# Kernel optimization log

Measured on AMD Instinct MI355X. Metric: run time of the kernel, lower is better.

Reference implementation:

```python
import jax, jax.numpy as jnp
import numpy as np

B, S, DIM = 2, 2048, 2048
NH, NKV = 16, 8
HD = DIM // NH  # 128
ROPE_THETA = 10000.0


def setup_inputs() -> dict:
    key = jax.random.key(0)
    ks = jax.random.split(key, 7)
    std = DIM ** -0.5
    x = jax.random.normal(ks[0], (B, S, DIM), jnp.float32)
    wq = jax.random.normal(ks[1], (NH * HD, DIM), jnp.float32) * std
    wk = jax.random.normal(ks[2], (NKV * HD, DIM), jnp.float32) * std
    wv = jax.random.normal(ks[3], (NKV * HD, DIM), jnp.float32) * std
    wo = jax.random.normal(ks[4], (DIM, NH * HD), jnp.float32) * std
    inv_freq = 1.0 / (ROPE_THETA ** (jnp.arange(0, HD, 2, dtype=jnp.float32) / HD))
    ang = jnp.arange(S, dtype=jnp.float32)[:, None] * inv_freq[None, :]  # [S, HD//2]
    freqs_cos = jnp.cos(ang)
    freqs_sin = jnp.sin(ang)
    # diffusion-style random per-batch token mask: t ~ U[0,1) per batch row
    t = jax.random.uniform(ks[5], (B, 1))
    mask = jax.random.uniform(ks[6], (B, S)) < t  # True = masked key
    mask = mask.at[:, 0].set(False)  # first token never masked
    return dict(x=x, wq=wq, wk=wk, wv=wv, wo=wo,
                freqs_cos=freqs_cos, freqs_sin=freqs_sin, mask=mask)


def _rope(x, cos, sin):
    # x: [b, s, h, d]; pairs (x[2i], x[2i+1]) rotated by angle[s, i]
    xr, xi = x[..., 0::2], x[..., 1::2]
    c = cos[None, :, None, :]
    s = sin[None, :, None, :]
    out = jnp.stack([xr * c - xi * s, xr * s + xi * c], axis=-1)
    return out.reshape(x.shape)


def reference(x, wq, wk, wv, wo, freqs_cos, freqs_sin, mask):
    b, s, _ = x.shape
    xq = jnp.einsum('bsd,ed->bse', x, wq).reshape(b, s, NH, HD)
    xk = jnp.einsum('bsd,ed->bse', x, wk).reshape(b, s, NKV, HD)
    xv = jnp.einsum('bsd,ed->bse', x, wv).reshape(b, s, NKV, HD)
    xq = _rope(xq, freqs_cos, freqs_sin)
    xk = _rope(xk, freqs_cos, freqs_sin)
    n_rep = NH // NKV
    xk = jnp.repeat(xk, n_rep, axis=2)  # repeat_kv (GQA)
    xv = jnp.repeat(xv, n_rep, axis=2)
    q = xq.transpose(0, 2, 1, 3)  # [b, h, s, d]
    k = xk.transpose(0, 2, 1, 3)
    v = xv.transpose(0, 2, 1, 3)
    scale = 1.0 / np.sqrt(HD).astype(np.float32)
    scores = jnp.einsum('bhqd,bhkd->bhqk', q, k) * scale  # [b, h, s, s]
    scores = jnp.where(mask[:, None, None, :], -jnp.inf, scores)
    probs = jax.nn.softmax(scores, axis=-1)
    out = jnp.einsum('bhqk,bhkd->bhqd', probs, v)
    out = out.transpose(0, 2, 1, 3).reshape(b, s, NH * HD)
    return jnp.einsum('bse,de->bsd', out, wo)
```

## Files before the change

kernel.cpp:

```cpp
#include <hip/hip_runtime.h>
#include <hip/hip_bf16.h>
#include <cstdint>
#include <cstddef>

#define S_LEN   2048
#define NHQ     16
#define NKV_H   8
#define HD_DIM  128
#define DMODEL  2048
#define BATCH   2
#define KVD     (NKV_H * HD_DIM)
#define QKV_LD  4096

typedef float f32x4  __attribute__((ext_vector_type(4)));
typedef __bf16 bf16x8 __attribute__((ext_vector_type(8)));
typedef __bf16 bf16x4 __attribute__((ext_vector_type(4)));

__device__ __forceinline__ void gload_lds16(const __bf16* g, __bf16* l) {
    __builtin_amdgcn_global_load_lds(
        (const __attribute__((address_space(1))) void*)g,
        (__attribute__((address_space(3))) void*)l, 16, 0, 0);
}

__global__ void sniff_x_kernel(const unsigned* __restrict__ x,
                               int* __restrict__ flag) {
    __shared__ int cnt;
    if (threadIdx.x == 0) cnt = 0;
    __syncthreads();
    int c = 0;
    for (int j = threadIdx.x; j < 1024; j += 256) {
        unsigned hw = x[j] & 0xFFFFu;
        unsigned e  = (hw >> 7) & 0xFF;
        if (hw == 0u || (e >= 118 && e <= 132)) c++;
    }
    atomicAdd(&cnt, c);
    __syncthreads();
    if (threadIdx.x == 0) *flag = (cnt > 512) ? 1 : 0;
}

__global__ void sniff_fc_kernel(const unsigned* __restrict__ fc,
                                int* __restrict__ flag) {
    if (threadIdx.x == 0) *flag = (fc[0] == 0x3F803F80u) ? 1 : 0;
}

__global__ void mask_norm_kernel(const unsigned char* __restrict__ mraw,
                                 unsigned char* __restrict__ mout, int n) {
    __shared__ int f_bf16, f_f32, f_u8;
    if (threadIdx.x == 0) { f_bf16 = 0; f_f32 = 0; f_u8 = 0; }
    __syncthreads();
    const unsigned* dw = (const unsigned*)mraw;
    int ndw = n / 4;
    for (int j = threadIdx.x; j < ndw; j += blockDim.x) {
        unsigned v = dw[j];
        if (v == 0x00003F80u || v == 0x3F803F80u) f_bf16 = 1;
        else if (v == 0x3F800000u) f_f32 = 1;
        else if (v & 0xFFFFFFFEu) f_u8 = 1;
    }
    __syncthreads();
    int layout;
    if (f_bf16) layout = 3;
    else if (f_f32) layout = 2;
    else if (f_u8) layout = 0;
    else layout = 1;
    for (int i = threadIdx.x; i < n; i += blockDim.x) {
        unsigned v;
        if (layout == 0)      v = mraw[i];
        else if (layout == 3) v = ((const unsigned short*)mraw)[i];
        else                  v = ((const unsigned*)mraw)[i];
        mout[i] = v ? 1u : 0u;
    }
}

__global__ __launch_bounds__(256)
void conv_bf16_kernel(const void* __restrict__ src, __bf16* __restrict__ dst,
                      int n8, const int* __restrict__ dflag) {
    int i = blockIdx.x * blockDim.x + threadIdx.x;
    if (i >= n8) return;
    size_t off = (size_t)i * 8;
    if (*dflag) {
        *reinterpret_cast<uint4*>(dst + off) =
            *reinterpret_cast<const uint4*>((const __bf16*)src + off);
    } else {
        const float* f = (const float*)src + off;
        float4 a = *reinterpret_cast<const float4*>(f);
        float4 b = *reinterpret_cast<const float4*>(f + 4);
        bf16x8 v;
        v[0] = (__bf16)a.x; v[1] = (__bf16)a.y; v[2] = (__bf16)a.z; v[3] = (__bf16)a.w;
        v[4] = (__bf16)b.x; v[5] = (__bf16)b.y; v[6] = (__bf16)b.z; v[7] = (__bf16)b.w;
        *reinterpret_cast<bf16x8*>(dst + off) = v;
    }
}

__global__ __launch_bounds__(256)
void conv_bf16_strided_kernel(const void* __restrict__ src,
                              __bf16* __restrict__ dstbase,
                              int n8, const int* __restrict__ dflag) {
    int i = blockIdx.x * blockDim.x + threadIdx.x;
    if (i >= n8) return;
    size_t off = (size_t)i * 8;
    size_t row = off >> 11;
    size_t col = off & 2047;
    __bf16* dst = dstbase + row * QKV_LD + col;
    if (*dflag) {
        *reinterpret_cast<uint4*>(dst) =
            *reinterpret_cast<const uint4*>((const __bf16*)src + off);
    } else {
        const float* f = (const float*)src + off;
        float4 a = *reinterpret_cast<const float4*>(f);
        float4 b = *reinterpret_cast<const float4*>(f + 4);
        bf16x8 v;
        v[0] = (__bf16)a.x; v[1] = (__bf16)a.y; v[2] = (__bf16)a.z; v[3] = (__bf16)a.w;
        v[4] = (__bf16)b.x; v[5] = (__bf16)b.y; v[6] = (__bf16)b.z; v[7] = (__bf16)b.w;
        *reinterpret_cast<bf16x8*>(dst) = v;
    }
}

template <bool OUT_BF16>
__global__ __launch_bounds__(256)
void gemm_bt_async(const __bf16* __restrict__ A, const __bf16* __restrict__ Bw,
                   void* __restrict__ Cv, int K, int lda, int ldb, int ldc) {
    __shared__ __align__(16) __bf16 As[128 * 64];
    __shared__ __align__(16) __bf16 Bs[128 * 64];

    const int t    = threadIdx.x;
    const int w    = t >> 6;
    const int lane = t & 63;
    const int quad = lane >> 4;
    const int l16  = lane & 15;
    const int wm   = (w >> 1) * 64;
    const int wn   = (w & 1) * 64;
    const int m0   = blockIdx.x * 128;
    const int n0   = blockIdx.y * 128;
    const int rl   = lane >> 3;
    const int gl   = lane & 7;

    f32x4 acc[4][4];
#pragma unroll
    for (int i = 0; i < 4; ++i)
#pragma unroll
        for (int j = 0; j < 4; ++j) acc[i][j] = (f32x4){0.f, 0.f, 0.f, 0.f};

    for (int k0 = 0; k0 < K; k0 += 64) {
        __syncthreads();
#pragma unroll
        for (int p = 0; p < 4; ++p) {
            const int rowb = w * 32 + p * 8;
            const int r    = rowb + rl;
            const int gA   = gl ^ rl;
            gload_lds16(A  + (size_t)(m0 + r) * lda + k0 + gA * 8, &As[rowb * 64]);
            gload_lds16(Bw + (size_t)(n0 + r) * ldb + k0 + gA * 8, &Bs[rowb * 64]);
        }
        __syncthreads();
#pragma unroll
        for (int ks = 0; ks < 2; ++ks) {
            const int G = ks * 4 + quad;
            const int gsw = (G ^ (l16 & 7)) * 8;
            bf16x8 af[4], bf[4];
#pragma unroll
            for (int i = 0; i < 4; ++i)
                af[i] = *reinterpret_cast<const bf16x8*>(
                    &As[(wm + i * 16 + l16) * 64 + gsw]);
#pragma unroll
            for (int j = 0; j < 4; ++j)
                bf[j] = *reinterpret_cast<const bf16x8*>(
                    &Bs[(wn + j * 16 + l16) * 64 + gsw]);
#pragma unroll
            for (int i = 0; i < 4; ++i)
#pragma unroll
                for (int j = 0; j < 4; ++j)
                    acc[i][j] = __builtin_amdgcn_mfma_f32_16x16x32_bf16(
                        af[i], bf[j], acc[i][j], 0, 0, 0);
        }
    }
#pragma unroll
    for (int i = 0; i < 4; ++i)
#pragma unroll
        for (int r = 0; r < 4; ++r) {
            size_t m = (size_t)(m0 + wm + i * 16 + quad * 4 + r);
#pragma unroll
            for (int j = 0; j < 4; ++j) {
                int n = n0 + wn + j * 16 + l16;
                if constexpr (OUT_BF16)
                    ((__hip_bfloat16*)Cv)[m * ldc + n] = __float2bfloat16(acc[i][j][r]);
                else
                    ((float*)Cv)[m * ldc + n] = acc[i][j][r];
            }
        }
}

__global__ void rope_kernel(__hip_bfloat16* __restrict__ xqk,
                            const void* __restrict__ cosv,
                            const void* __restrict__ sinv,
                            const int* __restrict__ dflag_fc,
                            int npairs) {
    int idx = blockIdx.x * blockDim.x + threadIdx.x;
    if (idx >= npairs) return;
    int i  = idx & 63;
    int h  = (idx >> 6) % 24;
    int bs = idx / (64 * 24);
    int s  = bs & (S_LEN - 1);
    float c, sn;
    if (*dflag_fc) {
        c  = __bfloat162float(((const __hip_bfloat16*)cosv)[s * 64 + i]);
        sn = __bfloat162float(((const __hip_bfloat16*)sinv)[s * 64 + i]);
    } else {
        c  = ((const float*)cosv)[s * 64 + i];
        sn = ((const float*)sinv)[s * 64 + i];
    }
    unsigned* p = (unsigned*)(xqk + (size_t)bs * QKV_LD + h * HD_DIM) + i;
    unsigned u = *p;
    float xr = __uint_as_float(u << 16);
    float xi = __uint_as_float(u & 0xFFFF0000u);
    float o0 = xr * c - xi * sn;
    float o1 = xr * sn + xi * c;
    union { __hip_bfloat16 h2[2]; unsigned u32; } out;
    out.h2[0] = __float2bfloat16(o0);
    out.h2[1] = __float2bfloat16(o1);
    *p = out.u32;
}

__global__ __launch_bounds__(256)
void transpose_v_kernel(const __hip_bfloat16* __restrict__ xv,
                        __hip_bfloat16* __restrict__ vt) {
    __shared__ unsigned short T[32][36];
    const int t  = threadIdx.x;
    const int s0 = blockIdx.x * 32;
    const int d0 = blockIdx.y * 32;
    const int z  = blockIdx.z;
    const int b  = z >> 3;
    const int kv = z & 7;
    {
        int sr = t >> 3, dc = (t & 7) * 4;
        const unsigned short* p = (const unsigned short*)xv
            + (size_t)(b * S_LEN + s0 + sr) * QKV_LD + kv * 128 + d0 + dc;
        uint2 v = *reinterpret_cast<const uint2*>(p);
        T[sr][dc + 0] = (unsigned short)(v.x & 0xFFFFu);
        T[sr][dc + 1] = (unsigned short)(v.x >> 16);
        T[sr][dc + 2] = (unsigned short)(v.y & 0xFFFFu);
        T[sr][dc + 3] = (unsigned short)(v.y >> 16);
    }
    __syncthreads();
    {
        int dr = t >> 3, sc = (t & 7) * 4;
        unsigned w0 = (unsigned)T[sc + 0][dr] | ((unsigned)T[sc + 1][dr] << 16);
        unsigned w1 = (unsigned)T[sc + 2][dr] | ((unsigned)T[sc + 3][dr] << 16);
        unsigned short* q = (unsigned short*)vt
            + ((size_t)z * 128 + d0 + dr) * S_LEN + s0 + sc;
        uint2 v; v.x = w0; v.y = w1;
        *reinterpret_cast<uint2*>(q) = v;
    }
}

__global__ __launch_bounds__(256)
void attn_mfma2_kernel(__hip_bfloat16* qkv,
                       const __hip_bfloat16* __restrict__ vt_g,
                       const unsigned char* __restrict__ msk) {
    __shared__ __align__(16) __bf16 Ks[64 * 128];
    __shared__ __align__(16) __bf16 Vt[128 * 64];
    __shared__ __align__(16) __bf16 Ps[4][16][64];

    const int t    = threadIdx.x;
    const int w    = t >> 6;
    const int lane = t & 63;
    const int quad = lane >> 4;
    const int l16  = lane & 15;

    const int bid = blockIdx.x;
    const int qt  = bid & 31;
    const int h   = (bid >> 5) & (NHQ - 1);
    const int b   = bid >> 9;
    const int kvh = h >> 1;
    const int q0  = qt * 64;

    bf16x8 qf[4];
    {
        const __bf16* qrow = (const __bf16*)qkv
            + (size_t)(b * S_LEN + q0 + w * 16 + l16) * QKV_LD + h * 128 + quad * 8;
#pragma unroll
        for (int ks = 0; ks < 4; ++ks)
            qf[ks] = *reinterpret_cast<const bf16x8*>(qrow + ks * 32);
    }

    float m_r = -INFINITY, l_r = 0.f;
    f32x4 o[8];
#pragma unroll
    for (int d0 = 0; d0 < 8; ++d0) o[d0] = (f32x4){0.f, 0.f, 0.f, 0.f};

    const float scale2 = 0.08838834764831845f * 1.4426950408889634f;

    const __bf16* xk = (const __bf16*)qkv + 2048;

    const int krl = lane >> 4, kgl = lane & 15;
    const int vrl = lane >> 3, vgl = lane & 7;
    const int gbase = lane & 48;

    for (int k0 = 0; k0 < S_LEN; k0 += 64) {
        __syncthreads();
#pragma unroll
        for (int p = 0; p < 4; ++p) {
            const int row  = w * 16 + p * 4 + krl;
            const int srcg = kgl ^ (row & 7);
            gload_lds16(xk + (size_t)(b * S_LEN + k0 + row) * QKV_LD
                            + kvh * 128 + srcg * 8,
                        &Ks[(w * 16 + p * 4) * 128]);
        }
#pragma unroll
        for (int p = 0; p < 4; ++p) {
            const int row  = w * 32 + p * 8 + vrl;
            const int srcg = vgl ^ (row & 7);
            gload_lds16((const __bf16*)vt_g
                            + ((size_t)(b * NKV_H + kvh) * 128 + row) * S_LEN
                            + k0 + srcg * 8,
                        &Vt[(w * 32 + p * 8) * 64]);
        }
        unsigned mk4[4];
        {
            const unsigned* mp = (const unsigned*)(msk + b * S_LEN + k0);
#pragma unroll
            for (int n0 = 0; n0 < 4; ++n0) mk4[n0] = mp[n0 * 4 + quad];
        }
        __syncthreads();

        f32x4 sc4[4];
#pragma unroll
        for (int n0 = 0; n0 < 4; ++n0) sc4[n0] = (f32x4){0.f, 0.f, 0.f, 0.f};
        __builtin_amdgcn_s_setprio(1);
#pragma unroll
        for (int ks = 0; ks < 4; ++ks) {
            const int G = ks * 4 + quad;
#pragma unroll
            for (int n0 = 0; n0 < 4; ++n0) {
                const int row  = n0 * 16 + l16;
                const int slot = G ^ (row & 7);
                bf16x8 kf = *reinterpret_cast<const bf16x8*>(&Ks[row * 128 + slot * 8]);
                sc4[n0] = __builtin_amdgcn_mfma_f32_16x16x32_bf16(kf, qf[ks], sc4[n0], 0, 0, 0);
            }
        }
        __builtin_amdgcn_s_setprio(0);

#pragma unroll
        for (int n0 = 0; n0 < 4; ++n0)
#pragma unroll
            for (int r = 0; r < 4; ++r)
                sc4[n0][r] = ((mk4[n0] >> (r * 8)) & 0xFF) ? -INFINITY : sc4[n0][r];

        float tq[4];
#pragma unroll
        for (int n0 = 0; n0 < 4; ++n0)
            tq[n0] = fmaxf(fmaxf(sc4[n0][0], sc4[n0][1]),
                           fmaxf(sc4[n0][2], sc4[n0][3]));
        float rm = fmaxf(fmaxf(tq[0], tq[1]), fmaxf(tq[2], tq[3]));
        rm = fmaxf(rm, __shfl_xor(rm, 16, 64));
        rm = fmaxf(rm, __shfl_xor(rm, 32, 64));

        bool need = (rm - m_r) * scale2 > 8.0f;
        if (__any((int)need)) {
            float mn = fmaxf(m_r, rm);
            float al = exp2f((m_r - mn) * scale2);
            m_r = mn;
            l_r *= al;
            float alq[4];
#pragma unroll
            for (int r = 0; r < 4; ++r)
                alq[r] = __shfl(al, gbase | (quad * 4 + r), 64);
#pragma unroll
            for (int d0 = 0; d0 < 8; ++d0)
#pragma unroll
                for (int r = 0; r < 4; ++r) o[d0][r] *= alq[r];
        }

        float negm = -m_r * scale2;
#pragma unroll
        for (int n0 = 0; n0 < 4; ++n0)
#pragma unroll
            for (int r = 0; r < 4; ++r) {
                float p = exp2f(fmaf(sc4[n0][r], scale2, negm));
                sc4[n0][r] = p;
                l_r += p;
            }

#pragma unroll
        for (int n0 = 0; n0 < 4; ++n0) {
            const int kb    = n0 * 16 + quad * 4;
            const int gran  = kb >> 3;
            const int half4 = kb & 4;
            const int slot  = gran ^ (l16 & 7);
            bf16x4 pk;
            pk[0] = (__bf16)sc4[n0][0];
            pk[1] = (__bf16)sc4[n0][1];
            pk[2] = (__bf16)sc4[n0][2];
            pk[3] = (__bf16)sc4[n0][3];
            *reinterpret_cast<bf16x4*>(&Ps[w][l16][slot * 8 + half4]) = pk;
        }

        __builtin_amdgcn_s_setprio(1);
#pragma unroll
        for (int kk = 0; kk < 64; kk += 32) {
            const int Gp    = (kk >> 3) + quad;
            const int slotp = Gp ^ (l16 & 7);
            bf16x8 af = *reinterpret_cast<const bf16x8*>(&Ps[w][l16][slotp * 8]);
#pragma unroll
            for (int d0 = 0; d0 < 8; ++d0) {
                const int row  = d0 * 16 + l16;
                const int slot = Gp ^ (row & 7);
                bf16x8 bf = *reinterpret_cast<const bf16x8*>(&Vt[row * 64 + slot * 8]);
                o[d0] = __builtin_amdgcn_mfma_f32_16x16x32_bf16(af, bf, o[d0], 0, 0, 0);
            }
        }
        __builtin_amdgcn_s_setprio(0);
    }

    float ls = l_r;
    ls += __shfl_xor(ls, 16, 64);
    ls += __shfl_xor(ls, 32, 64);
    float invl = 1.f / ls;
    float invq[4];
#pragma unroll
    for (int r = 0; r < 4; ++r)
        invq[r] = __shfl(invl, gbase | (quad * 4 + r), 64);
    __hip_bfloat16* att = qkv;
#pragma unroll
    for (int d0 = 0; d0 < 8; ++d0)
#pragma unroll
        for (int r = 0; r < 4; ++r) {
            size_t row = (size_t)(b * S_LEN + q0 + w * 16 + quad * 4 + r);
            att[row * QKV_LD + h * 128 + d0 * 16 + l16] =
                __float2bfloat16(o[d0][r] * invq[r]);
        }
}

extern "C" void kernel_launch(void* const* d_in, const int* in_sizes, int n_in,
                              void* d_out, int out_size, void* d_ws, size_t ws_size,
                              hipStream_t stream) {
    const void* x  = d_in[0];
    const void* wq = d_in[1];
    const void* wk = d_in[2];
    const void* wv = d_in[3];
    const void* wo = d_in[4];
    const void* fc = d_in[5];
    const void* fs = d_in[6];
    const unsigned char* mraw = (const unsigned char*)d_in[7];

    const int M = BATCH * S_LEN;
    char* wsb = (char*)d_ws;
    int* dflag_x  = (int*)wsb;
    int* dflag_fc = (int*)(wsb + 64);
    unsigned char* mnorm = (unsigned char*)(wsb + 128);
    __hip_bfloat16* qkv = (__hip_bfloat16*)(wsb + 8192);

    char* dob = (char*)d_out;
    __bf16* xb    = (__bf16*)dob;
    __bf16* wcomb = (__bf16*)(dob + (16u << 20));
    __bf16* wqb = wcomb;
    __bf16* wkb = wcomb + (size_t)2048 * 2048;
    __bf16* wvb = wcomb + (size_t)3072 * 2048;
    __hip_bfloat16* vt = (__hip_bfloat16*)d_out;

    hipLaunchKernelGGL(sniff_x_kernel, dim3(1), dim3(256), 0, stream,
                       (const unsigned*)x, dflag_x);
    hipLaunchKernelGGL(sniff_fc_kernel, dim3(1), dim3(64), 0, stream,
                       (const unsigned*)fc, dflag_fc);
    hipLaunchKernelGGL(mask_norm_kernel, dim3(1), dim3(256), 0, stream,
                       mraw, mnorm, BATCH * S_LEN);

    hipLaunchKernelGGL(conv_bf16_kernel, dim3((M * DMODEL / 8) / 256), dim3(256), 0, stream,
                       x, xb, M * DMODEL / 8, dflag_x);
    hipLaunchKernelGGL(conv_bf16_kernel, dim3((DMODEL * DMODEL / 8) / 256), dim3(256), 0, stream,
                       wq, wqb, DMODEL * DMODEL / 8, dflag_x);
    hipLaunchKernelGGL(conv_bf16_kernel, dim3((KVD * DMODEL / 8) / 256), dim3(256), 0, stream,
                       wk, wkb, KVD * DMODEL / 8, dflag_x);
    hipLaunchKernelGGL(conv_bf16_kernel, dim3((KVD * DMODEL / 8) / 256), dim3(256), 0, stream,
                       wv, wvb, KVD * DMODEL / 8, dflag_x);

    hipLaunchKernelGGL((gemm_bt_async<true>), dim3(M / 128, QKV_LD / 128), dim3(256), 0, stream,
                       xb, wcomb, (void*)qkv, DMODEL, DMODEL, DMODEL, QKV_LD);

    int npairs = M * 24 * (HD_DIM / 2);
    hipLaunchKernelGGL(rope_kernel, dim3(npairs / 256), dim3(256), 0, stream,
                       qkv, fc, fs, dflag_fc, npairs);

    hipLaunchKernelGGL(transpose_v_kernel, dim3(S_LEN / 32, HD_DIM / 32, BATCH * NKV_H),
                       dim3(256), 0, stream, qkv + 3072, vt);

    hipLaunchKernelGGL(attn_mfma2_kernel, dim3(BATCH * NHQ * (S_LEN / 64)), dim3(256), 0, stream,
                       qkv, vt, mnorm);

    hipLaunchKernelGGL(conv_bf16_strided_kernel, dim3((DMODEL * DMODEL / 8) / 256), dim3(256), 0, stream,
                       wo, (__bf16*)qkv + 2048, DMODEL * DMODEL / 8, dflag_x);

    hipLaunchKernelGGL((gemm_bt_async<false>), dim3(M / 128, DMODEL / 128), dim3(256), 0, stream,
                       (const __bf16*)qkv, (const __bf16*)qkv + 2048, d_out,
                       DMODEL, QKV_LD, QKV_LD, DMODEL);
}
```

Measured before the change: 434.6 us.

## Double-buffer attention K/V tiles, swizzle block order, merge prep and convert launches

The attention kernel now double-buffers its K and V LDS tiles, issuing async global-to-LDS loads for the next tile while the current one is computed. This drops one barrier per iteration and hides load latency. The GEMM and attention grids get an XCD-aware block-index swizzle so neighbouring tiles share L2. The three sniff/mask kernels are fused into one launch, as are the four bf16 conversion kernels, to cut launch overhead. LDS use for attention roughly doubles for K/V, which may lower occupancy.

New measurement: 432.4 us. No clear change (-0.5%).

```diff
diff --git a/kernel.cpp b/kernel.cpp
--- a/kernel.cpp
+++ b/kernel.cpp
@@ -22,62 +22,57 @@
         (__attribute__((address_space(3))) void*)l, 16, 0, 0);
 }
 
-__global__ void sniff_x_kernel(const unsigned* __restrict__ x,
-                               int* __restrict__ flag) {
-    __shared__ int cnt;
-    if (threadIdx.x == 0) cnt = 0;
-    __syncthreads();
-    int c = 0;
-    for (int j = threadIdx.x; j < 1024; j += 256) {
-        unsigned hw = x[j] & 0xFFFFu;
-        unsigned e  = (hw >> 7) & 0xFF;
-        if (hw == 0u || (e >= 118 && e <= 132)) c++;
-    }
-    atomicAdd(&cnt, c);
-    __syncthreads();
-    if (threadIdx.x == 0) *flag = (cnt > 512) ? 1 : 0;
-}
-
-__global__ void sniff_fc_kernel(const unsigned* __restrict__ fc,
-                                int* __restrict__ flag) {
-    if (threadIdx.x == 0) *flag = (fc[0] == 0x3F803F80u) ? 1 : 0;
-}
-
-__global__ void mask_norm_kernel(const unsigned char* __restrict__ mraw,
-                                 unsigned char* __restrict__ mout, int n) {
-    __shared__ int f_bf16, f_f32, f_u8;
-    if (threadIdx.x == 0) { f_bf16 = 0; f_f32 = 0; f_u8 = 0; }
-    __syncthreads();
-    const unsigned* dw = (const unsigned*)mraw;
-    int ndw = n / 4;
-    for (int j = threadIdx.x; j < ndw; j += blockDim.x) {
-        unsigned v = dw[j];
-        if (v == 0x00003F80u || v == 0x3F803F80u) f_bf16 = 1;
-        else if (v == 0x3F800000u) f_f32 = 1;
-        else if (v & 0xFFFFFFFEu) f_u8 = 1;
-    }
-    __syncthreads();
-    int layout;
-    if (f_bf16) layout = 3;
-    else if (f_f32) layout = 2;
-    else if (f_u8) layout = 0;
-    else layout = 1;
-    for (int i = threadIdx.x; i < n; i += blockDim.x) {
-        unsigned v;
-        if (layout == 0)      v = mraw[i];
-        else if (layout == 3) v = ((const unsigned short*)mraw)[i];
-        else                  v = ((const unsigned*)mraw)[i];
-        mout[i] = v ? 1u : 0u;
-    }
-}
-
 __global__ __launch_bounds__(256)
-void conv_bf16_kernel(const void* __restrict__ src, __bf16* __restrict__ dst,
-                      int n8, const int* __restrict__ dflag) {
-    int i = blockIdx.x * blockDim.x + threadIdx.x;
-    if (i >= n8) return;
-    size_t off = (size_t)i * 8;
-    if (*dflag) {
+void prep_kernel(const unsigned* __restrict__ x, int* __restrict__ flag_x,
+                 const unsigned* __restrict__ fc, int* __restrict__ flag_fc,
+                 const unsigned char* __restrict__ mraw,
+                 unsigned char* __restrict__ mout, int n) {
+    if (blockIdx.x == 0) {
+        __shared__ int cnt;
+        if (threadIdx.x == 0) cnt = 0;
+        __syncthreads();
+        int c = 0;
+        for (int j = threadIdx.x; j < 1024; j += 256) {
+            unsigned hw = x[j] & 0xFFFFu;
+            unsigned e  = (hw >> 7) & 0xFF;
+            if (hw == 0u || (e >= 118 && e <= 132)) c++;
+        }
+        atomicAdd(&cnt, c);
+        __syncthreads();
+        if (threadIdx.x == 0) *flag_x = (cnt > 512) ? 1 : 0;
+    } else if (blockIdx.x == 1) {
+        if (threadIdx.x == 0) *flag_fc = (fc[0] == 0x3F803F80u) ? 1 : 0;
+    } else {
+        __shared__ int f_bf16, f_f32, f_u8;
+        if (threadIdx.x == 0) { f_bf16 = 0; f_f32 = 0; f_u8 = 0; }
+        __syncthreads();
+        const unsigned* dw = (const unsigned*)mraw;
+        int ndw = n / 4;
+        for (int j = threadIdx.x; j < ndw; j += blockDim.x) {
+            unsigned v = dw[j];
+            if (v == 0x00003F80u || v == 0x3F803F80u) f_bf16 = 1;
+            else if (v == 0x3F800000u) f_f32 = 1;
+            else if (v & 0xFFFFFFFEu) f_u8 = 1;
+        }
+        __syncthreads();
+        int layout;
+        if (f_bf16) layout = 3;
+        else if (f_f32) layout = 2;
+        else if (f_u8) layout = 0;
+        else layout = 1;
+        for (int i = threadIdx.x; i < n; i += blockDim.x) {
+            unsigned v;
+            if (layout == 0)      v = mraw[i];
+            else if (layout == 3) v = ((const unsigned short*)mraw)[i];
+            else                  v = ((const unsigned*)mraw)[i];
+            mout[i] = v ? 1u : 0u;
+        }
+    }
+}
+
+__device__ __forceinline__ void conv8(const void* src, __bf16* dst,
+                                      size_t off, int isbf16) {
+    if (isbf16) {
         *reinterpret_cast<uint4*>(dst + off) =
             *reinterpret_cast<const uint4*>((const __bf16*)src + off);
     } else {
@@ -88,6 +83,24 @@
         v[0] = (__bf16)a.x; v[1] = (__bf16)a.y; v[2] = (__bf16)a.z; v[3] = (__bf16)a.w;
         v[4] = (__bf16)b.x; v[5] = (__bf16)b.y; v[6] = (__bf16)b.z; v[7] = (__bf16)b.w;
         *reinterpret_cast<bf16x8*>(dst + off) = v;
+    }
+}
+
+__global__ __launch_bounds__(256)
+void conv_all_kernel(const void* __restrict__ x,  const void* __restrict__ wq,
+                     const void* __restrict__ wk, const void* __restrict__ wv,
+                     __bf16* __restrict__ xb, __bf16* __restrict__ wcomb,
+                     const int* __restrict__ dflag) {
+    int i = blockIdx.x * 256 + threadIdx.x;
+    int isb = *dflag;
+    if (i < 1048576) {
+        conv8(x, xb, (size_t)i * 8, isb);
+    } else if (i < 1572864) {
+        conv8(wq, wcomb, (size_t)(i - 1048576) * 8, isb);
+    } else if (i < 1835008) {
+        conv8(wk, wcomb + (size_t)2048 * 2048, (size_t)(i - 1572864) * 8, isb);
+    } else {
+        conv8(wv, wcomb + (size_t)3072 * 2048, (size_t)(i - 1835008) * 8, isb);
     }
 }
 
@@ -129,8 +142,13 @@
     const int l16  = lane & 15;
     const int wm   = (w >> 1) * 64;
     const int wn   = (w & 1) * 64;
-    const int m0   = blockIdx.x * 128;
-    const int n0   = blockIdx.y * 128;
+
+    const int nwg  = gridDim.x * gridDim.y;
+    const int lin  = blockIdx.y * gridDim.x + blockIdx.x;
+    const int swz  = (lin & 7) * (nwg >> 3) + (lin >> 3);
+    const int m0   = (swz % gridDim.x) * 128;
+    const int n0   = (swz / gridDim.x) * 128;
+
     const int rl   = lane >> 3;
     const int gl   = lane & 7;
 
@@ -255,8 +273,8 @@
 void attn_mfma2_kernel(__hip_bfloat16* qkv,
                        const __hip_bfloat16* __restrict__ vt_g,
                        const unsigned char* __restrict__ msk) {
-    __shared__ __align__(16) __bf16 Ks[64 * 128];
-    __shared__ __align__(16) __bf16 Vt[128 * 64];
+    __shared__ __align__(16) __bf16 Ks[2][64 * 128];
+    __shared__ __align__(16) __bf16 Vt[2][128 * 64];
     __shared__ __align__(16) __bf16 Ps[4][16][64];
 
     const int t    = threadIdx.x;
@@ -265,7 +283,7 @@
     const int quad = lane >> 4;
     const int l16  = lane & 15;
 
-    const int bid = blockIdx.x;
+    const int bid = ((blockIdx.x & 7) << 7) | (blockIdx.x >> 3);
     const int qt  = bid & 31;
     const int h   = (bid >> 5) & (NHQ - 1);
     const int b   = bid >> 9;
@@ -287,39 +305,52 @@
     for (int d0 = 0; d0 < 8; ++d0) o[d0] = (f32x4){0.f, 0.f, 0.f, 0.f};
 
     const float scale2 = 0.08838834764831845f * 1.4426950408889634f;
-
-    const __bf16* xk = (const __bf16*)qkv + 2048;
-
-    const int krl = lane >> 4, kgl = lane & 15;
-    const int vrl = lane >> 3, vgl = lane & 7;
     const int gbase = lane & 48;
 
-    for (int k0 = 0; k0 < S_LEN; k0 += 64) {
-        __syncthreads();
+    const __bf16* kp[4];
+    const __bf16* vp[4];
+    {
+        const __bf16* xk = (const __bf16*)qkv + 2048;
+        const int krl = lane >> 4, kgl = lane & 15;
+        const int vrl = lane >> 3, vgl = lane & 7;
 #pragma unroll
         for (int p = 0; p < 4; ++p) {
-            const int row  = w * 16 + p * 4 + krl;
-            const int srcg = kgl ^ (row & 7);
-            gload_lds16(xk + (size_t)(b * S_LEN + k0 + row) * QKV_LD
-                            + kvh * 128 + srcg * 8,
-                        &Ks[(w * 16 + p * 4) * 128]);
+            const int row = w * 16 + p * 4 + krl;
+            kp[p] = xk + (size_t)(b * S_LEN + row) * QKV_LD
+                       + kvh * 128 + (kgl ^ (row & 7)) * 8;
         }
 #pragma unroll
         for (int p = 0; p < 4; ++p) {
-            const int row  = w * 32 + p * 8 + vrl;
-            const int srcg = vgl ^ (row & 7);
-            gload_lds16((const __bf16*)vt_g
-                            + ((size_t)(b * NKV_H + kvh) * 128 + row) * S_LEN
-                            + k0 + srcg * 8,
-                        &Vt[(w * 32 + p * 8) * 64]);
-        }
+            const int row = w * 32 + p * 8 + vrl;
+            vp[p] = (const __bf16*)vt_g
+                  + ((size_t)(b * NKV_H + kvh) * 128 + row) * S_LEN
+                  + (vgl ^ (row & 7)) * 8;
+        }
+    }
+    const unsigned char* mbase = msk + b * S_LEN;
+
+    auto stage = [&](int sb) {
+#pragma unroll
+        for (int p = 0; p < 4; ++p) {
+            gload_lds16(kp[p], &Ks[sb][(w * 16 + p * 4) * 128]);
+            kp[p] += 64 * QKV_LD;
+        }
+#pragma unroll
+        for (int p = 0; p < 4; ++p) {
+            gload_lds16(vp[p], &Vt[sb][(w * 32 + p * 8) * 64]);
+            vp[p] += 64;
+        }
+    };
+
+    auto tile_body = [&](int kmask, int cb, int sb, bool do_stage) {
+        if (do_stage) stage(sb);
+
         unsigned mk4[4];
         {
-            const unsigned* mp = (const unsigned*)(msk + b * S_LEN + k0);
+            const unsigned* mp = (const unsigned*)(mbase + kmask);
 #pragma unroll
             for (int n0 = 0; n0 < 4; ++n0) mk4[n0] = mp[n0 * 4 + quad];
         }
-        __syncthreads();
 
         f32x4 sc4[4];
 #pragma unroll
@@ -332,7 +363,7 @@
             for (int n0 = 0; n0 < 4; ++n0) {
                 const int row  = n0 * 16 + l16;
                 const int slot = G ^ (row & 7);
-                bf16x8 kf = *reinterpret_cast<const bf16x8*>(&Ks[row * 128 + slot * 8]);
+                bf16x8 kf = *reinterpret_cast<const bf16x8*>(&Ks[cb][row * 128 + slot * 8]);
                 sc4[n0] = __builtin_amdgcn_mfma_f32_16x16x32_bf16(kf, qf[ks], sc4[n0], 0, 0, 0);
             }
         }
@@ -403,11 +434,21 @@
             for (int d0 = 0; d0 < 8; ++d0) {
                 const int row  = d0 * 16 + l16;
                 const int slot = Gp ^ (row & 7);
-                bf16x8 bf = *reinterpret_cast<const bf16x8*>(&Vt[row * 64 + slot * 8]);
+                bf16x8 bf = *reinterpret_cast<const bf16x8*>(&Vt[cb][row * 64 + slot * 8]);
                 o[d0] = __builtin_amdgcn_mfma_f32_16x16x32_bf16(af, bf, o[d0], 0, 0, 0);
             }
         }
         __builtin_amdgcn_s_setprio(0);
+
+        __syncthreads();
+    };
+
+    stage(0);
+    __syncthreads();
+
+    for (int k0 = 0; k0 < S_LEN; k0 += 128) {
+        tile_body(k0,      0, 1, true);
+        tile_body(k0 + 64, 1, 0, k0 + 128 < S_LEN);
     }
 
     float ls = l_r;
@@ -451,26 +492,14 @@
     char* dob = (char*)d_out;
     __bf16* xb    = (__bf16*)dob;
     __bf16* wcomb = (__bf16*)(dob + (16u << 20));
-    __bf16* wqb = wcomb;
-    __bf16* wkb = wcomb + (size_t)2048 * 2048;
-    __bf16* wvb = wcomb + (size_t)3072 * 2048;
     __hip_bfloat16* vt = (__hip_bfloat16*)d_out;
 
-    hipLaunchKernelGGL(sniff_x_kernel, dim3(1), dim3(256), 0, stream,
-                       (const unsigned*)x, dflag_x);
-    hipLaunchKernelGGL(sniff_fc_kernel, dim3(1), dim3(64), 0, stream,
-                       (const unsigned*)fc, dflag_fc);
-    hipLaunchKernelGGL(mask_norm_kernel, dim3(1), dim3(256), 0, stream,
+    hipLaunchKernelGGL(prep_kernel, dim3(3), dim3(256), 0, stream,
+                       (const unsigned*)x, dflag_x, (const unsigned*)fc, dflag_fc,
                        mraw, mnorm, BATCH * S_LEN);
 
-    hipLaunchKernelGGL(conv_bf16_kernel, dim3((M * DMODEL / 8) / 256), dim3(256), 0, stream,
-                       x, xb, M * DMODEL / 8, dflag_x);
-    hipLaunchKernelGGL(conv_bf16_kernel, dim3((DMODEL * DMODEL / 8) / 256), dim3(256), 0, stream,
-                       wq, wqb, DMODEL * DMODEL / 8, dflag_x);
-    hipLaunchKernelGGL(conv_bf16_kernel, dim3((KVD * DMODEL / 8) / 256), dim3(256), 0, stream,
-                       wk, wkb, KVD * DMODEL / 8, dflag_x);
-    hipLaunchKernelGGL(conv_bf16_kernel, dim3((KVD * DMODEL / 8) / 256), dim3(256), 0, stream,
-                       wv, wvb, KVD * DMODEL / 8, dflag_x);
+    hipLaunchKernelGGL(conv_all_kernel, dim3(8192), dim3(256), 0, stream,
+                       x, wq, wk, wv, xb, wcomb, dflag_x);
 
     hipLaunchKernelGGL((gemm_bt_async<true>), dim3(M / 128, QKV_LD / 128), dim3(256), 0, stream,
                        xb, wcomb, (void*)qkv, DMODEL, DMODEL, DMODEL, QKV_LD);
```
